# Kernel optimization log

Measured on AMD Instinct MI355X. Metric: run time of the kernel, lower is better.

## Reference

```python
import jax, jax.numpy as jnp
import numpy as np

B, H, L, T, V, LAYERS = 512, 256, 256, 64, 128, 2
SOS = 0


def setup_inputs() -> dict:
    key = jax.random.key(0)
    ks = jax.random.split(key, 10)
    s = 0.05
    return {
        "x": jax.random.normal(ks[0], (B, H, 1, L), jnp.float32),          # encoder memory
        "y": jax.random.randint(ks[1], (B, T), 0, V, jnp.int32),            # teacher tokens
        "emb": jax.random.normal(ks[2], (V, H), jnp.float32) * s,           # embedding table
        "attn_w": jax.random.normal(ks[3], (L, 2 * H), jnp.float32) * s,    # attn Linear [out,in]
        "attn_b": jnp.zeros((L,), jnp.float32),
        "comb_w": jax.random.normal(ks[4], (H, 2 * H), jnp.float32) * s,    # attn_combine
        "comb_b": jnp.zeros((H,), jnp.float32),
        "gru_w_ih": jax.random.normal(ks[5], (LAYERS, 3 * H, H), jnp.float32) * s,
        "gru_w_hh": jax.random.normal(ks[6], (LAYERS, 3 * H, H), jnp.float32) * s,
        "gru_b_ih": jnp.zeros((LAYERS, 3 * H), jnp.float32),
        "gru_b_hh": jnp.zeros((LAYERS, 3 * H), jnp.float32),
        "out_w": jax.random.normal(ks[7], (V, H), jnp.float32) * s,
        "out_b": jnp.zeros((V,), jnp.float32),
    }


def reference(x, y, emb, attn_w, attn_b, comb_w, comb_b,
              gru_w_ih, gru_w_hh, gru_b_ih, gru_b_hh, out_w, out_b):
    # x: [B, H, 1, L] -> encoder memory enc: [B, L, H]
    enc = jnp.transpose(x[:, :, 0, :], (0, 2, 1))
    b = x.shape[0]
    h0 = jnp.zeros((LAYERS, b, H), x.dtype)
    # teacher forcing: input at step t is y[:, t-1], with SOS at t=0
    tokens = jnp.concatenate([jnp.full((b, 1), SOS, y.dtype), y[:, :-1]], axis=1)  # [B, T]

    def step(hidden, tok):
        e = emb[tok]  # [B, H] (dropout disabled / eval mode)
        scores = jnp.concatenate([e, hidden[0]], axis=1) @ attn_w.T + attn_b  # [B, L]
        aw = jax.nn.softmax(scores, axis=1)
        applied = jnp.einsum('bl,blh->bh', aw, enc)  # [B, H]
        g = jax.nn.relu(jnp.concatenate([applied, e], axis=1) @ comb_w.T + comb_b)
        xin = g
        hs = []
        for l in range(LAYERS):  # single-step multilayer GRU (PyTorch equations)
            gi = xin @ gru_w_ih[l].T + gru_b_ih[l]
            gh = hidden[l] @ gru_w_hh[l].T + gru_b_hh[l]
            ir, iz, inn = jnp.split(gi, 3, axis=1)
            hr, hz, hn = jnp.split(gh, 3, axis=1)
            r = jax.nn.sigmoid(ir + hr)
            z = jax.nn.sigmoid(iz + hz)
            n = jnp.tanh(inn + r * hn)
            hnew = (1 - z) * n + z * hidden[l]
            hs.append(hnew)
            xin = hnew
        logp = jax.nn.log_softmax(xin @ out_w.T + out_b, axis=1)  # [B, V]
        return jnp.stack(hs), (logp, aw)

    _, (outs, attns) = jax.lax.scan(step, h0, tokens.T)  # outs: [T,B,V], attns: [T,B,L]
    return jnp.transpose(outs, (1, 2, 0)), jnp.transpose(attns, (1, 0, 2))
```

## Files before the change

### kernel.cpp

```cpp
#include <hip/hip_runtime.h>
#include <math.h>

#define B 512
#define H 256
#define L 256
#define T 64
#define V 128
#define LAYERS 2
#define SOS 0

#define OFF_A 0
#define OFF_C 131072
#define OFF_G 262144
#define GRU_LAYER_STRIDE (6 * 65536)
#define GRU_MAT_STRIDE 65536
#define OFF_O (OFF_G + LAYERS * GRU_LAYER_STRIDE)
#define WS_HALVES (OFF_O + 32768)
#define OFF_XT WS_HALVES
#define XT_B_STRIDE (32 * 256 * 8)
#define XT_HALVES ((size_t)B * XT_B_STRIDE)
#define WS_NEED_BYTES ((size_t)(OFF_XT + XT_HALVES) * 2)

typedef _Float16 half8 __attribute__((ext_vector_type(8)));
typedef _Float16 half2t __attribute__((ext_vector_type(2)));
typedef unsigned int u32x4 __attribute__((ext_vector_type(4)));
typedef float f32x4 __attribute__((ext_vector_type(4)));

__device__ __forceinline__ float fdot2(half2t a, half2t b, float c) {
#if __has_builtin(__builtin_amdgcn_fdot2)
    return __builtin_amdgcn_fdot2(a, b, c, false);
#else
    return c + (float)a[0] * (float)b[0] + (float)a[1] * (float)b[1];
#endif
}

union H8 {
    half8 v;
    half2t p[4];
    u32x4 u;
};

__device__ __forceinline__ half8 nt_load_h8(const _Float16* p) {
    H8 t;
    t.u = __builtin_nontemporal_load((const u32x4*)p);
    return t.v;
}

__device__ __forceinline__ float sigmoidf_(float v) {
    return 1.f / (1.f + __expf(-v));
}
__device__ __forceinline__ float fast_tanh(float v) {
    v = fminf(fmaxf(v, -15.f), 15.f);
    float e = __expf(-2.f * v);
    return (1.f - e) / (1.f + e);
}

__global__ void prep_pack(const float* __restrict__ attn_w,
                          const float* __restrict__ comb_w,
                          const float* __restrict__ gru_w_ih,
                          const float* __restrict__ gru_w_hh,
                          const float* __restrict__ out_w,
                          _Float16* __restrict__ ws) {
    int stride = gridDim.x * blockDim.x;
    for (int idx = blockIdx.x * blockDim.x + threadIdx.x; idx < WS_HALVES; idx += stride) {
        float val;
        if (idx < OFF_C) {
            int i = idx & 7, r = idx >> 3;
            int l = r & 255, k8 = r >> 8;
            val = attn_w[l * 512 + k8 * 8 + i];
        } else if (idx < OFF_G) {
            int e = idx - OFF_C;
            int i = e & 7, r = e >> 3;
            int hh = r & 255, k8 = r >> 8;
            val = comb_w[hh * 512 + k8 * 8 + i];
        } else if (idx < OFF_O) {
            int e = idx - OFF_G;
            int layer = e / GRU_LAYER_STRIDE;
            e -= layer * GRU_LAYER_STRIDE;
            int mat = e >> 16;
            e &= 65535;
            int i = e & 7, r = e >> 3;
            int j = r & 255, k8 = r >> 8;
            int k = k8 * 8 + i;
            const float* src = (mat < 3) ? gru_w_ih : gru_w_hh;
            int gate = (mat < 3) ? mat : mat - 3;
            val = src[layer * (768 * 256) + (gate * 256 + j) * 256 + k];
        } else {
            int e = idx - OFF_O;
            int i = e & 7, r = e >> 3;
            int v = r & 127, k8 = r >> 7;
            val = out_w[v * 256 + k8 * 8 + i];
        }
        ws[idx] = (_Float16)val;
    }
}

__global__ void prep_x(const float* __restrict__ x, _Float16* __restrict__ xt) {
    const int b = blockIdx.x;
    const int h = threadIdx.x;
    const float* xr = x + ((size_t)b * H + h) * L;
    _Float16* base = xt + (size_t)b * XT_B_STRIDE + h * 8;
#pragma unroll 4
    for (int k8 = 0; k8 < 32; ++k8) {
        float4 v0 = *(const float4*)(xr + k8 * 8);
        float4 v1 = *(const float4*)(xr + k8 * 8 + 4);
        half8 o;
        o[0] = (_Float16)v0.x; o[1] = (_Float16)v0.y;
        o[2] = (_Float16)v0.z; o[3] = (_Float16)v0.w;
        o[4] = (_Float16)v1.x; o[5] = (_Float16)v1.y;
        o[6] = (_Float16)v1.z; o[7] = (_Float16)v1.w;
        *(half8*)(base + k8 * 2048) = o;
    }
}

template <bool USE_XT>
__global__ __launch_bounds__(1024, 4) void decoder_kernel(
    const float* __restrict__ x,
    const int* __restrict__ y,
    const float* __restrict__ emb,
    const float* __restrict__ attn_b,
    const float* __restrict__ comb_b,
    const float* __restrict__ gru_b_ih,
    const float* __restrict__ gru_b_hh,
    const float* __restrict__ out_b,
    const _Float16* __restrict__ wsh,
    const _Float16* __restrict__ xt,
    float* __restrict__ out) {
    __shared__ __align__(16) _Float16 ehf[2][512];
    __shared__ __align__(16) _Float16 hfs[LAYERS][2][256];
    __shared__ __align__(16) float h32[LAYERS][2][256];
    __shared__ __align__(16) _Float16 apf[2][256];
    __shared__ __align__(16) _Float16 gfv[2][256];
    __shared__ __align__(16) _Float16 awf[2][256];
    __shared__ __align__(16) float aw32[2][256];
    __shared__ __align__(16) float pbuf[4][2][256];
    __shared__ __align__(16) float pgru[4][2][3][256];
    __shared__ __align__(16) float po[4][2][128];
    __shared__ __align__(16) float lgbuf[2][128][33];

    const int tid = threadIdx.x;
    const int G = tid >> 8;
    const int h = tid & 255;
    const int lane = tid & 63;
    const int w = tid >> 6;
    const int b0 = blockIdx.x * 2;

    const _Float16* AW = wsh + OFF_A;
    const _Float16* CW = wsh + OFF_C;
    const _Float16* OW = wsh + OFF_O;

    const float ab = attn_b[h];
    const float cb = comb_b[h];
    const float ob = out_b[h & 127];
    float b_ir[LAYERS], b_iz[LAYERS], b_in[LAYERS], b_hr[LAYERS], b_hz[LAYERS], b_hn[LAYERS];
#pragma unroll
    for (int l = 0; l < LAYERS; ++l) {
        b_ir[l] = gru_b_ih[l * 768 + h];
        b_iz[l] = gru_b_ih[l * 768 + 256 + h];
        b_in[l] = gru_b_ih[l * 768 + 512 + h];
        b_hr[l] = gru_b_hh[l * 768 + h];
        b_hz[l] = gru_b_hh[l * 768 + 256 + h];
        b_hn[l] = gru_b_hh[l * 768 + 512 + h];
    }

    if (G < 2) {
#pragma unroll
        for (int l = 0; l < LAYERS; ++l) {
            h32[l][G][h] = 0.f;
            hfs[l][G][h] = (_Float16)0.f;
        }
        ehf[G][256 + h] = (_Float16)0.f;
    }
    __syncthreads();

    for (int t = 0; t < T; ++t) {
        if (G < 2) {
            int tok = (t == 0) ? SOS : y[(b0 + G) * T + (t - 1)];
            ehf[G][h] = (_Float16)emb[tok * H + h];
        }
        __syncthreads();

        {
            float a00 = 0.f, a01 = 0.f, a10 = 0.f, a11 = 0.f;
            const _Float16* wp = AW + ((G * 16) << 11) + (h << 3);
            const _Float16* e0 = &ehf[0][G << 7];
            const _Float16* e1 = &ehf[1][G << 7];
#pragma unroll 4
            for (int k8 = 0; k8 < 16; ++k8) {
                H8 uw, u0, u1;
                uw.v = *(const half8*)(wp + (k8 << 11));
                u0.v = *(const half8*)(e0 + (k8 << 3));
                u1.v = *(const half8*)(e1 + (k8 << 3));
                a00 = fdot2(uw.p[0], u0.p[0], a00);
                a00 = fdot2(uw.p[1], u0.p[1], a00);
                a01 = fdot2(uw.p[2], u0.p[2], a01);
                a01 = fdot2(uw.p[3], u0.p[3], a01);
                a10 = fdot2(uw.p[0], u1.p[0], a10);
                a10 = fdot2(uw.p[1], u1.p[1], a10);
                a11 = fdot2(uw.p[2], u1.p[2], a11);
                a11 = fdot2(uw.p[3], u1.p[3], a11);
            }
            float bias = (G == 0) ? ab : 0.f;
            pbuf[G][0][h] = a00 + a01 + bias;
            pbuf[G][1][h] = a10 + a11 + bias;
        }
        __syncthreads();

        if (w < 2) {
            const int r = w;
            float s0 = pbuf[0][r][lane] + pbuf[1][r][lane] + pbuf[2][r][lane] + pbuf[3][r][lane];
            float s1 = pbuf[0][r][lane + 64] + pbuf[1][r][lane + 64] + pbuf[2][r][lane + 64] + pbuf[3][r][lane + 64];
            float s2 = pbuf[0][r][lane + 128] + pbuf[1][r][lane + 128] + pbuf[2][r][lane + 128] + pbuf[3][r][lane + 128];
            float s3 = pbuf[0][r][lane + 192] + pbuf[1][r][lane + 192] + pbuf[2][r][lane + 192] + pbuf[3][r][lane + 192];
            float m = fmaxf(fmaxf(s0, s1), fmaxf(s2, s3));
            for (int off = 32; off; off >>= 1) m = fmaxf(m, __shfl_xor(m, off));
            float e0 = __expf(s0 - m), e1 = __expf(s1 - m);
            float e2 = __expf(s2 - m), e3 = __expf(s3 - m);
            float s = e0 + e1 + e2 + e3;
            for (int off = 32; off; off >>= 1) s += __shfl_xor(s, off);
            float inv = 1.f / s;
            e0 *= inv; e1 *= inv; e2 *= inv; e3 *= inv;
            if (USE_XT) {
                awf[r][lane] = (_Float16)e0;
                awf[r][lane + 64] = (_Float16)e1;
                awf[r][lane + 128] = (_Float16)e2;
                awf[r][lane + 192] = (_Float16)e3;
            } else {
                aw32[r][lane] = e0;
                aw32[r][lane + 64] = e1;
                aw32[r][lane + 128] = e2;
                aw32[r][lane + 192] = e3;
            }
            float* outA = out + (size_t)B * V * T + ((size_t)(b0 + r) * T + t) * L;
            __builtin_nontemporal_store(e0, outA + lane);
            __builtin_nontemporal_store(e1, outA + lane + 64);
            __builtin_nontemporal_store(e2, outA + lane + 128);
            __builtin_nontemporal_store(e3, outA + lane + 192);
        }
        __syncthreads();

        {
            const int r = G & 1;
            const int q = G >> 1;
            if (USE_XT) {
                const _Float16* xrow = xt + (size_t)(b0 + r) * XT_B_STRIDE + (q << 15) + (h << 3);
                const _Float16* ap = &awf[r][q << 7];
                float a0 = 0.f, a1 = 0.f;
#pragma unroll 4
                for (int k8 = 0; k8 < 16; ++k8) {
                    H8 uw, ua;
                    uw.v = nt_load_h8(xrow + (k8 << 11));
                    ua.v = *(const half8*)(ap + (k8 << 3));
                    a0 = fdot2(uw.p[0], ua.p[0], a0);
                    a0 = fdot2(uw.p[1], ua.p[1], a0);
                    a1 = fdot2(uw.p[2], ua.p[2], a1);
                    a1 = fdot2(uw.p[3], ua.p[3], a1);
                }
                pbuf[G][0][h] = a0 + a1;
            } else {
                const float* xrow = x + ((size_t)(b0 + r) * H + h) * L + (q << 7);
                const float* ap = &aw32[r][q << 7];
                float a0 = 0.f, a1 = 0.f;
#pragma unroll 4
                for (int l = 0; l < 128; l += 8) {
                    float4 x0 = *(const float4*)(xrow + l);
                    float4 x1 = *(const float4*)(xrow + l + 4);
                    float4 w0 = *(const float4*)(ap + l);
                    float4 w1 = *(const float4*)(ap + l + 4);
                    a0 += x0.x * w0.x + x0.y * w0.y + x0.z * w0.z + x0.w * w0.w;
                    a1 += x1.x * w1.x + x1.y * w1.y + x1.z * w1.z + x1.w * w1.w;
                }
                pbuf[G][0][h] = a0 + a1;
            }
        }
        __syncthreads();

        if (G < 2) apf[G][h] = (_Float16)(pbuf[G][0][h] + pbuf[G + 2][0][h]);
        __syncthreads();

        {
            float a00 = 0.f, a01 = 0.f, a10 = 0.f, a11 = 0.f;
            const _Float16* wp = CW + ((G * 16) << 11) + (h << 3);
            const _Float16* i0 = (G < 2) ? &apf[0][G << 7] : &ehf[0][(G - 2) << 7];
            const _Float16* i1 = (G < 2) ? &apf[1][G << 7] : &ehf[1][(G - 2) << 7];
#pragma unroll 4
            for (int k8 = 0; k8 < 16; ++k8) {
                H8 uw, u0, u1;
                uw.v = *(const half8*)(wp + (k8 << 11));
                u0.v = *(const half8*)(i0 + (k8 << 3));
                u1.v = *(const half8*)(i1 + (k8 << 3));
                a00 = fdot2(uw.p[0], u0.p[0], a00);
                a00 = fdot2(uw.p[1], u0.p[1], a00);
                a01 = fdot2(uw.p[2], u0.p[2], a01);
                a01 = fdot2(uw.p[3], u0.p[3], a01);
                a10 = fdot2(uw.p[0], u1.p[0], a10);
                a10 = fdot2(uw.p[1], u1.p[1], a10);
                a11 = fdot2(uw.p[2], u1.p[2], a11);
                a11 = fdot2(uw.p[3], u1.p[3], a11);
            }
            pbuf[G][0][h] = a00 + a01;
            pbuf[G][1][h] = a10 + a11;
        }
        __syncthreads();
        if (G < 2)
            gfv[G][h] = (_Float16)fmaxf(
                pbuf[0][G][h] + pbuf[1][G][h] + pbuf[2][G][h] + pbuf[3][G][h] + cb, 0.f);
        __syncthreads();

#pragma unroll
        for (int layer = 0; layer < LAYERS; ++layer) {
            const int mh = G >> 1;
            const int kq = G & 1;
            const _Float16* GW = wsh + OFF_G + layer * GRU_LAYER_STRIDE +
                                 mh * 3 * GRU_MAT_STRIDE + ((kq * 16) << 11) + (h << 3);
            const _Float16* act0;
            const _Float16* act1;
            if (mh == 0) {
                act0 = ((layer == 0) ? &gfv[0][0] : &hfs[0][0][0]) + (kq << 7);
                act1 = ((layer == 0) ? &gfv[1][0] : &hfs[0][1][0]) + (kq << 7);
            } else {
                act0 = &hfs[layer][0][0] + (kq << 7);
                act1 = &hfs[layer][1][0] + (kq << 7);
            }
            float aA0 = 0.f, aB0 = 0.f, aC0 = 0.f, aA1 = 0.f, aB1 = 0.f, aC1 = 0.f;
#pragma unroll 4
            for (int k8 = 0; k8 < 16; ++k8) {
                H8 w0, w1, w2, u0, u1;
                const int off = k8 << 11;
                w0.v = *(const half8*)(GW + off);
                w1.v = *(const half8*)(GW + GRU_MAT_STRIDE + off);
                w2.v = *(const half8*)(GW + 2 * GRU_MAT_STRIDE + off);
                u0.v = *(const half8*)(act0 + (k8 << 3));
                u1.v = *(const half8*)(act1 + (k8 << 3));
#pragma unroll
                for (int p = 0; p < 4; ++p) {
                    aA0 = fdot2(w0.p[p], u0.p[p], aA0);
                    aB0 = fdot2(w1.p[p], u0.p[p], aB0);
                    aC0 = fdot2(w2.p[p], u0.p[p], aC0);
                    aA1 = fdot2(w0.p[p], u1.p[p], aA1);
                    aB1 = fdot2(w1.p[p], u1.p[p], aB1);
                    aC1 = fdot2(w2.p[p], u1.p[p], aC1);
                }
            }
            pgru[G][0][0][h] = aA0;
            pgru[G][0][1][h] = aB0;
            pgru[G][0][2][h] = aC0;
            pgru[G][1][0][h] = aA1;
            pgru[G][1][1][h] = aB1;
            pgru[G][1][2][h] = aC1;
            __syncthreads();
            if (G < 2) {
                const int r = G;
                float gi_r = pgru[0][r][0][h] + pgru[1][r][0][h];
                float gi_z = pgru[0][r][1][h] + pgru[1][r][1][h];
                float gi_n = pgru[0][r][2][h] + pgru[1][r][2][h];
                float gh_r = pgru[2][r][0][h] + pgru[3][r][0][h];
                float gh_z = pgru[2][r][1][h] + pgru[3][r][1][h];
                float gh_n = pgru[2][r][2][h] + pgru[3][r][2][h];
                float rr = sigmoidf_(gi_r + b_ir[layer] + gh_r + b_hr[layer]);
                float zz = sigmoidf_(gi_z + b_iz[layer] + gh_z + b_hz[layer]);
                float nn = fast_tanh(gi_n + b_in[layer] + rr * (gh_n + b_hn[layer]));
                float hnew = (1.f - zz) * nn + zz * h32[layer][r][h];
                h32[layer][r][h] = hnew;
                hfs[layer][r][h] = (_Float16)hnew;
                if (layer == 0) ehf[r][256 + h] = (_Float16)hnew;
            }
            __syncthreads();
        }

        {
            const int v = h & 127;
            const int r = h >> 7;
            const _Float16* hp = &hfs[1][r][0] + (G << 6);
            const _Float16* wp = OW + ((G * 8) << 10) + (v << 3);
            float a0 = 0.f, a1 = 0.f;
#pragma unroll 4
            for (int k8 = 0; k8 < 8; ++k8) {
                H8 uw, ua;
                uw.v = *(const half8*)(wp + (k8 << 10));
                ua.v = *(const half8*)(hp + (k8 << 3));
                a0 = fdot2(uw.p[0], ua.p[0], a0);
                a0 = fdot2(uw.p[1], ua.p[1], a0);
                a1 = fdot2(uw.p[2], ua.p[2], a1);
                a1 = fdot2(uw.p[3], ua.p[3], a1);
            }
            po[G][r][v] = a0 + a1 + ((G == 0) ? ob : 0.f);
        }
        __syncthreads();

        if (w < 2) {
            const int r = w;
            float l0 = po[0][r][lane] + po[1][r][lane] + po[2][r][lane] + po[3][r][lane];
            float l1 = po[0][r][lane + 64] + po[1][r][lane + 64] + po[2][r][lane + 64] + po[3][r][lane + 64];
            float m = fmaxf(l0, l1);
            for (int off = 32; off; off >>= 1) m = fmaxf(m, __shfl_xor(m, off));
            float s = __expf(l0 - m) + __expf(l1 - m);
            for (int off = 32; off; off >>= 1) s += __shfl_xor(s, off);
            float lse = m + __logf(s);
            lgbuf[r][lane][t & 31] = l0 - lse;
            lgbuf[r][lane + 64][t & 31] = l1 - lse;
        }

        if ((t & 31) == 31) {
            __syncthreads();
            const int tb = t & ~31;
#pragma unroll
            for (int c = 0; c < 2; ++c) {
                int fidx = c * 1024 + tid;
                int r = fidx >> 10;
                int rem = fidx & 1023;
                int v = rem >> 3;
                int tq = (rem & 7) << 2;
                f32x4 vec = {lgbuf[r][v][tq], lgbuf[r][v][tq + 1],
                             lgbuf[r][v][tq + 2], lgbuf[r][v][tq + 3]};
                float* dst = out + (size_t)(b0 + r) * V * T + (size_t)v * T + tb + tq;
                __builtin_nontemporal_store(vec, (f32x4*)dst);
            }
        }
    }
}

extern "C" void kernel_launch(void* const* d_in, const int* in_sizes, int n_in,
                              void* d_out, int out_size, void* d_ws, size_t ws_size,
                              hipStream_t stream) {
    const float* x = (const float*)d_in[0];
    const int* y = (const int*)d_in[1];
    const float* emb = (const float*)d_in[2];
    const float* attn_w = (const float*)d_in[3];
    const float* attn_b = (const float*)d_in[4];
    const float* comb_w = (const float*)d_in[5];
    const float* comb_b = (const float*)d_in[6];
    const float* gru_w_ih = (const float*)d_in[7];
    const float* gru_w_hh = (const float*)d_in[8];
    const float* gru_b_ih = (const float*)d_in[9];
    const float* gru_b_hh = (const float*)d_in[10];
    const float* out_w = (const float*)d_in[11];
    const float* out_b = (const float*)d_in[12];
    float* out = (float*)d_out;
    _Float16* ws = (_Float16*)d_ws;

    prep_pack<<<512, 256, 0, stream>>>(attn_w, comb_w, gru_w_ih, gru_w_hh, out_w, ws);
    if (ws_size >= WS_NEED_BYTES) {
        _Float16* xt = ws + OFF_XT;
        prep_x<<<B, 256, 0, stream>>>(x, xt);
        decoder_kernel<true><<<B / 2, 1024, 0, stream>>>(
            x, y, emb, attn_b, comb_b, gru_b_ih, gru_b_hh, out_b, ws, xt, out);
    } else {
        decoder_kernel<false><<<B / 2, 1024, 0, stream>>>(
            x, y, emb, attn_b, comb_b, gru_b_ih, gru_b_hh, out_b, ws, nullptr, out);
    }
}
```

Measured before the change: 2.087 ms.

## Process four batch rows per block to reuse weight loads across rows

Each workgroup now handles four sequences instead of two, so every packed fp16 weight vector loaded for the attention, combine, GRU and output projections is reused across four activation rows. Grid size halves to 128 blocks. The attention-apply step is reassigned so each 256-thread group covers a full row over all of L, which removes one reduction pass and a barrier. Costs are more LDS, more accumulator registers per thread, and fewer blocks than CUs, which can leave compute units idle. The logits flush now runs every 8 steps instead of every 32, and the host-side argument variables were shuffled, though the values passed stay the same.

```diff
diff --git a/kernel.cpp b/kernel.cpp
--- a/kernel.cpp
+++ b/kernel.cpp
@@ -126,24 +126,24 @@
     const _Float16* __restrict__ wsh,
     const _Float16* __restrict__ xt,
     float* __restrict__ out) {
-    __shared__ __align__(16) _Float16 ehf[2][512];
-    __shared__ __align__(16) _Float16 hfs[LAYERS][2][256];
-    __shared__ __align__(16) float h32[LAYERS][2][256];
-    __shared__ __align__(16) _Float16 apf[2][256];
-    __shared__ __align__(16) _Float16 gfv[2][256];
-    __shared__ __align__(16) _Float16 awf[2][256];
-    __shared__ __align__(16) float aw32[2][256];
-    __shared__ __align__(16) float pbuf[4][2][256];
-    __shared__ __align__(16) float pgru[4][2][3][256];
-    __shared__ __align__(16) float po[4][2][128];
-    __shared__ __align__(16) float lgbuf[2][128][33];
+    __shared__ __align__(16) _Float16 ehf[4][512];
+    __shared__ __align__(16) _Float16 hfs[LAYERS][4][256];
+    __shared__ __align__(16) float h32[LAYERS][4][256];
+    __shared__ __align__(16) _Float16 apf[4][256];
+    __shared__ __align__(16) _Float16 gfv[4][256];
+    __shared__ __align__(16) _Float16 awf[4][256];
+    __shared__ __align__(16) float aw32[4][256];
+    __shared__ __align__(16) float pbuf[4][4][256];
+    __shared__ __align__(16) float pgru[4][4][3][256];
+    __shared__ __align__(16) float po[4][4][128];
+    __shared__ __align__(16) float lgbuf[4][128][9];
 
     const int tid = threadIdx.x;
     const int G = tid >> 8;
     const int h = tid & 255;
     const int lane = tid & 63;
     const int w = tid >> 6;
-    const int b0 = blockIdx.x * 2;
+    const int b0 = blockIdx.x * 4;
 
     const _Float16* AW = wsh + OFF_A;
     const _Float16* CW = wsh + OFF_C;
@@ -151,7 +151,7 @@
 
     const float ab = attn_b[h];
     const float cb = comb_b[h];
-    const float ob = out_b[h & 127];
+    const float ob = out_b[tid & 127];
     float b_ir[LAYERS], b_iz[LAYERS], b_in[LAYERS], b_hr[LAYERS], b_hz[LAYERS], b_hn[LAYERS];
 #pragma unroll
     for (int l = 0; l < LAYERS; ++l) {
@@ -163,50 +163,53 @@
         b_hn[l] = gru_b_hh[l * 768 + 512 + h];
     }
 
-    if (G < 2) {
-#pragma unroll
-        for (int l = 0; l < LAYERS; ++l) {
-            h32[l][G][h] = 0.f;
-            hfs[l][G][h] = (_Float16)0.f;
-        }
-        ehf[G][256 + h] = (_Float16)0.f;
-    }
+#pragma unroll
+    for (int l = 0; l < LAYERS; ++l) {
+        h32[l][G][h] = 0.f;
+        hfs[l][G][h] = (_Float16)0.f;
+    }
+    ehf[G][256 + h] = (_Float16)0.f;
     __syncthreads();
 
     for (int t = 0; t < T; ++t) {
-        if (G < 2) {
+        {
             int tok = (t == 0) ? SOS : y[(b0 + G) * T + (t - 1)];
             ehf[G][h] = (_Float16)emb[tok * H + h];
         }
         __syncthreads();
 
         {
-            float a00 = 0.f, a01 = 0.f, a10 = 0.f, a11 = 0.f;
+            float a0 = 0.f, a1 = 0.f, a2 = 0.f, a3 = 0.f;
             const _Float16* wp = AW + ((G * 16) << 11) + (h << 3);
             const _Float16* e0 = &ehf[0][G << 7];
             const _Float16* e1 = &ehf[1][G << 7];
+            const _Float16* e2 = &ehf[2][G << 7];
+            const _Float16* e3 = &ehf[3][G << 7];
 #pragma unroll 4
             for (int k8 = 0; k8 < 16; ++k8) {
-                H8 uw, u0, u1;
+                H8 uw, u0, u1, u2, u3;
                 uw.v = *(const half8*)(wp + (k8 << 11));
                 u0.v = *(const half8*)(e0 + (k8 << 3));
                 u1.v = *(const half8*)(e1 + (k8 << 3));
-                a00 = fdot2(uw.p[0], u0.p[0], a00);
-                a00 = fdot2(uw.p[1], u0.p[1], a00);
-                a01 = fdot2(uw.p[2], u0.p[2], a01);
-                a01 = fdot2(uw.p[3], u0.p[3], a01);
-                a10 = fdot2(uw.p[0], u1.p[0], a10);
-                a10 = fdot2(uw.p[1], u1.p[1], a10);
-                a11 = fdot2(uw.p[2], u1.p[2], a11);
-                a11 = fdot2(uw.p[3], u1.p[3], a11);
+                u2.v = *(const half8*)(e2 + (k8 << 3));
+                u3.v = *(const half8*)(e3 + (k8 << 3));
+#pragma unroll
+                for (int p = 0; p < 4; ++p) {
+                    a0 = fdot2(uw.p[p], u0.p[p], a0);
+                    a1 = fdot2(uw.p[p], u1.p[p], a1);
+                    a2 = fdot2(uw.p[p], u2.p[p], a2);
+                    a3 = fdot2(uw.p[p], u3.p[p], a3);
+                }
             }
             float bias = (G == 0) ? ab : 0.f;
-            pbuf[G][0][h] = a00 + a01 + bias;
-            pbuf[G][1][h] = a10 + a11 + bias;
-        }
-        __syncthreads();
-
-        if (w < 2) {
+            pbuf[G][0][h] = a0 + bias;
+            pbuf[G][1][h] = a1 + bias;
+            pbuf[G][2][h] = a2 + bias;
+            pbuf[G][3][h] = a3 + bias;
+        }
+        __syncthreads();
+
+        if (w < 4) {
             const int r = w;
             float s0 = pbuf[0][r][lane] + pbuf[1][r][lane] + pbuf[2][r][lane] + pbuf[3][r][lane];
             float s1 = pbuf[0][r][lane + 64] + pbuf[1][r][lane + 64] + pbuf[2][r][lane + 64] + pbuf[3][r][lane + 64];
@@ -239,72 +242,69 @@
         }
         __syncthreads();
 
+        if (USE_XT) {
+            const _Float16* xrow = xt + (size_t)(b0 + G) * XT_B_STRIDE + (h << 3);
+            const _Float16* ap = &awf[G][0];
+            float a0 = 0.f, a1 = 0.f;
+#pragma unroll 4
+            for (int k8 = 0; k8 < 32; ++k8) {
+                H8 uw, ua;
+                uw.v = nt_load_h8(xrow + (k8 << 11));
+                ua.v = *(const half8*)(ap + (k8 << 3));
+                a0 = fdot2(uw.p[0], ua.p[0], a0);
+                a0 = fdot2(uw.p[1], ua.p[1], a0);
+                a1 = fdot2(uw.p[2], ua.p[2], a1);
+                a1 = fdot2(uw.p[3], ua.p[3], a1);
+            }
+            apf[G][h] = (_Float16)(a0 + a1);
+        } else {
+            const float* xrow = x + ((size_t)(b0 + G) * H + h) * L;
+            const float* ap = &aw32[G][0];
+            float a0 = 0.f, a1 = 0.f;
+#pragma unroll 4
+            for (int l = 0; l < L; l += 8) {
+                float4 x0 = *(const float4*)(xrow + l);
+                float4 x1 = *(const float4*)(xrow + l + 4);
+                float4 w0 = *(const float4*)(ap + l);
+                float4 w1 = *(const float4*)(ap + l + 4);
+                a0 += x0.x * w0.x + x0.y * w0.y + x0.z * w0.z + x0.w * w0.w;
+                a1 += x1.x * w1.x + x1.y * w1.y + x1.z * w1.z + x1.w * w1.w;
+            }
+            apf[G][h] = (_Float16)(a0 + a1);
+        }
+        __syncthreads();
+
         {
-            const int r = G & 1;
-            const int q = G >> 1;
-            if (USE_XT) {
-                const _Float16* xrow = xt + (size_t)(b0 + r) * XT_B_STRIDE + (q << 15) + (h << 3);
-                const _Float16* ap = &awf[r][q << 7];
-                float a0 = 0.f, a1 = 0.f;
-#pragma unroll 4
-                for (int k8 = 0; k8 < 16; ++k8) {
-                    H8 uw, ua;
-                    uw.v = nt_load_h8(xrow + (k8 << 11));
-                    ua.v = *(const half8*)(ap + (k8 << 3));
-                    a0 = fdot2(uw.p[0], ua.p[0], a0);
-                    a0 = fdot2(uw.p[1], ua.p[1], a0);
-                    a1 = fdot2(uw.p[2], ua.p[2], a1);
-                    a1 = fdot2(uw.p[3], ua.p[3], a1);
-                }
-                pbuf[G][0][h] = a0 + a1;
-            } else {
-                const float* xrow = x + ((size_t)(b0 + r) * H + h) * L + (q << 7);
-                const float* ap = &aw32[r][q << 7];
-                float a0 = 0.f, a1 = 0.f;
-#pragma unroll 4
-                for (int l = 0; l < 128; l += 8) {
-                    float4 x0 = *(const float4*)(xrow + l);
-                    float4 x1 = *(const float4*)(xrow + l + 4);
-                    float4 w0 = *(const float4*)(ap + l);
-                    float4 w1 = *(const float4*)(ap + l + 4);
-                    a0 += x0.x * w0.x + x0.y * w0.y + x0.z * w0.z + x0.w * w0.w;
-                    a1 += x1.x * w1.x + x1.y * w1.y + x1.z * w1.z + x1.w * w1.w;
-                }
-                pbuf[G][0][h] = a0 + a1;
-            }
-        }
-        __syncthreads();
-
-        if (G < 2) apf[G][h] = (_Float16)(pbuf[G][0][h] + pbuf[G + 2][0][h]);
-        __syncthreads();
-
-        {
-            float a00 = 0.f, a01 = 0.f, a10 = 0.f, a11 = 0.f;
+            float a0 = 0.f, a1 = 0.f, a2 = 0.f, a3 = 0.f;
             const _Float16* wp = CW + ((G * 16) << 11) + (h << 3);
             const _Float16* i0 = (G < 2) ? &apf[0][G << 7] : &ehf[0][(G - 2) << 7];
             const _Float16* i1 = (G < 2) ? &apf[1][G << 7] : &ehf[1][(G - 2) << 7];
+            const _Float16* i2 = (G < 2) ? &apf[2][G << 7] : &ehf[2][(G - 2) << 7];
+            const _Float16* i3 = (G < 2) ? &apf[3][G << 7] : &ehf[3][(G - 2) << 7];
 #pragma unroll 4
             for (int k8 = 0; k8 < 16; ++k8) {
-                H8 uw, u0, u1;
+                H8 uw, u0, u1, u2, u3;
                 uw.v = *(const half8*)(wp + (k8 << 11));
                 u0.v = *(const half8*)(i0 + (k8 << 3));
                 u1.v = *(const half8*)(i1 + (k8 << 3));
-                a00 = fdot2(uw.p[0], u0.p[0], a00);
-                a00 = fdot2(uw.p[1], u0.p[1], a00);
-                a01 = fdot2(uw.p[2], u0.p[2], a01);
-                a01 = fdot2(uw.p[3], u0.p[3], a01);
-                a10 = fdot2(uw.p[0], u1.p[0], a10);
-                a10 = fdot2(uw.p[1], u1.p[1], a10);
-                a11 = fdot2(uw.p[2], u1.p[2], a11);
-                a11 = fdot2(uw.p[3], u1.p[3], a11);
-            }
-            pbuf[G][0][h] = a00 + a01;
-            pbuf[G][1][h] = a10 + a11;
-        }
-        __syncthreads();
-        if (G < 2)
-            gfv[G][h] = (_Float16)fmaxf(
-                pbuf[0][G][h] + pbuf[1][G][h] + pbuf[2][G][h] + pbuf[3][G][h] + cb, 0.f);
+                u2.v = *(const half8*)(i2 + (k8 << 3));
+                u3.v = *(const half8*)(i3 + (k8 << 3));
+#pragma unroll
+                for (int p = 0; p < 4; ++p) {
+                    a0 = fdot2(uw.p[p], u0.p[p], a0);
+                    a1 = fdot2(uw.p[p], u1.p[p], a1);
+                    a2 = fdot2(uw.p[p], u2.p[p], a2);
+                    a3 = fdot2(uw.p[p], u3.p[p], a3);
+                }
+            }
+            pbuf[G][0][h] = a0;
+            pbuf[G][1][h] = a1;
+            pbuf[G][2][h] = a2;
+            pbuf[G][3][h] = a3;
+        }
+        __syncthreads();
+        gfv[G][h] = (_Float16)fmaxf(
+            pbuf[0][G][h] + pbuf[1][G][h] + pbuf[2][G][h] + pbuf[3][G][h] + cb, 0.f);
         __syncthreads();
 
 #pragma unroll
@@ -313,43 +313,44 @@
             const int kq = G & 1;
             const _Float16* GW = wsh + OFF_G + layer * GRU_LAYER_STRIDE +
                                  mh * 3 * GRU_MAT_STRIDE + ((kq * 16) << 11) + (h << 3);
-            const _Float16* act0;
-            const _Float16* act1;
-            if (mh == 0) {
-                act0 = ((layer == 0) ? &gfv[0][0] : &hfs[0][0][0]) + (kq << 7);
-                act1 = ((layer == 0) ? &gfv[1][0] : &hfs[0][1][0]) + (kq << 7);
-            } else {
-                act0 = &hfs[layer][0][0] + (kq << 7);
-                act1 = &hfs[layer][1][0] + (kq << 7);
-            }
-            float aA0 = 0.f, aB0 = 0.f, aC0 = 0.f, aA1 = 0.f, aB1 = 0.f, aC1 = 0.f;
-#pragma unroll 4
+            const _Float16* act[4];
+#pragma unroll
+            for (int r = 0; r < 4; ++r) {
+                if (mh == 0)
+                    act[r] = ((layer == 0) ? &gfv[r][0] : &hfs[0][r][0]) + (kq << 7);
+                else
+                    act[r] = &hfs[layer][r][0] + (kq << 7);
+            }
+            float aA[4] = {0.f, 0.f, 0.f, 0.f};
+            float aB[4] = {0.f, 0.f, 0.f, 0.f};
+            float aC[4] = {0.f, 0.f, 0.f, 0.f};
+#pragma unroll 2
             for (int k8 = 0; k8 < 16; ++k8) {
-                H8 w0, w1, w2, u0, u1;
+                H8 w0, w1, w2, u[4];
                 const int off = k8 << 11;
                 w0.v = *(const half8*)(GW + off);
                 w1.v = *(const half8*)(GW + GRU_MAT_STRIDE + off);
                 w2.v = *(const half8*)(GW + 2 * GRU_MAT_STRIDE + off);
-                u0.v = *(const half8*)(act0 + (k8 << 3));
-                u1.v = *(const half8*)(act1 + (k8 << 3));
+#pragma unroll
+                for (int r = 0; r < 4; ++r) u[r].v = *(const half8*)(act[r] + (k8 << 3));
 #pragma unroll
                 for (int p = 0; p < 4; ++p) {
-                    aA0 = fdot2(w0.p[p], u0.p[p], aA0);
-                    aB0 = fdot2(w1.p[p], u0.p[p], aB0);
-                    aC0 = fdot2(w2.p[p], u0.p[p], aC0);
-                    aA1 = fdot2(w0.p[p], u1.p[p], aA1);
-                    aB1 = fdot2(w1.p[p], u1.p[p], aB1);
-                    aC1 = fdot2(w2.p[p], u1.p[p], aC1);
+#pragma unroll
+                    for (int r = 0; r < 4; ++r) {
+                        aA[r] = fdot2(w0.p[p], u[r].p[p], aA[r]);
+                        aB[r] = fdot2(w1.p[p], u[r].p[p], aB[r]);
+                        aC[r] = fdot2(w2.p[p], u[r].p[p], aC[r]);
+                    }
                 }
             }
-            pgru[G][0][0][h] = aA0;
-            pgru[G][0][1][h] = aB0;
-            pgru[G][0][2][h] = aC0;
-            pgru[G][1][0][h] = aA1;
-            pgru[G][1][1][h] = aB1;
-            pgru[G][1][2][h] = aC1;
+#pragma unroll
+            for (int r = 0; r < 4; ++r) {
+                pgru[G][r][0][h] = aA[r];
+                pgru[G][r][1][h] = aB[r];
+                pgru[G][r][2][h] = aC[r];
+            }
             __syncthreads();
-            if (G < 2) {
+            {
                 const int r = G;
                 float gi_r = pgru[0][r][0][h] + pgru[1][r][0][h];
                 float gi_z = pgru[0][r][1][h] + pgru[1][r][1][h];
@@ -368,27 +369,36 @@
             __syncthreads();
         }
 
-        {
-            const int v = h & 127;
-            const int r = h >> 7;
-            const _Float16* hp = &hfs[1][r][0] + (G << 6);
-            const _Float16* wp = OW + ((G * 8) << 10) + (v << 3);
-            float a0 = 0.f, a1 = 0.f;
-#pragma unroll 4
+        if (tid < 512) {
+            const int v = tid & 127;
+            const int kq = tid >> 7;
+            const _Float16* wp = OW + ((kq * 8) << 10) + (v << 3);
+            float a0 = 0.f, a1 = 0.f, a2 = 0.f, a3 = 0.f;
+#pragma unroll 2
             for (int k8 = 0; k8 < 8; ++k8) {
-                H8 uw, ua;
+                H8 uw, u0, u1, u2, u3;
                 uw.v = *(const half8*)(wp + (k8 << 10));
-                ua.v = *(const half8*)(hp + (k8 << 3));
-                a0 = fdot2(uw.p[0], ua.p[0], a0);
-                a0 = fdot2(uw.p[1], ua.p[1], a0);
-                a1 = fdot2(uw.p[2], ua.p[2], a1);
-                a1 = fdot2(uw.p[3], ua.p[3], a1);
-            }
-            po[G][r][v] = a0 + a1 + ((G == 0) ? ob : 0.f);
-        }
-        __syncthreads();
-
-        if (w < 2) {
+                u0.v = *(const half8*)(&hfs[1][0][kq << 6] + (k8 << 3));
+                u1.v = *(const half8*)(&hfs[1][1][kq << 6] + (k8 << 3));
+                u2.v = *(const half8*)(&hfs[1][2][kq << 6] + (k8 << 3));
+                u3.v = *(const half8*)(&hfs[1][3][kq << 6] + (k8 << 3));
+#pragma unroll
+                for (int p = 0; p < 4; ++p) {
+                    a0 = fdot2(uw.p[p], u0.p[p], a0);
+                    a1 = fdot2(uw.p[p], u1.p[p], a1);
+                    a2 = fdot2(uw.p[p], u2.p[p], a2);
+                    a3 = fdot2(uw.p[p], u3.p[p], a3);
+                }
+            }
+            float bias = (kq == 0) ? ob : 0.f;
+            po[kq][0][v] = a0 + bias;
+            po[kq][1][v] = a1 + bias;
+            po[kq][2][v] = a2 + bias;
+            po[kq][3][v] = a3 + bias;
+        }
+        __syncthreads();
+
+        if (w < 4) {
             const int r = w;
             float l0 = po[0][r][lane] + po[1][r][lane] + po[2][r][lane] + po[3][r][lane];
             float l1 = po[0][r][lane + 64] + po[1][r][lane + 64] + po[2][r][lane + 64] + po[3][r][lane + 64];
@@ -397,25 +407,21 @@
             float s = __expf(l0 - m) + __expf(l1 - m);
             for (int off = 32; off; off >>= 1) s += __shfl_xor(s, off);
             float lse = m + __logf(s);
-            lgbuf[r][lane][t & 31] = l0 - lse;
-            lgbuf[r][lane + 64][t & 31] = l1 - lse;
-        }
-
-        if ((t & 31) == 31) {
+            lgbuf[r][lane][t & 7] = l0 - lse;
+            lgbuf[r][lane + 64][t & 7] = l1 - lse;
+        }
+
+        if ((t & 7) == 7) {
             __syncthreads();
-            const int tb = t & ~31;
-#pragma unroll
-            for (int c = 0; c < 2; ++c) {
-                int fidx = c * 1024 + tid;
-                int r = fidx >> 10;
-                int rem = fidx & 1023;
-                int v = rem >> 3;
-                int tq = (rem & 7) << 2;
-                f32x4 vec = {lgbuf[r][v][tq], lgbuf[r][v][tq + 1],
-                             lgbuf[r][v][tq + 2], lgbuf[r][v][tq + 3]};
-                float* dst = out + (size_t)(b0 + r) * V * T + (size_t)v * T + tb + tq;
-                __builtin_nontemporal_store(vec, (f32x4*)dst);
-            }
+            const int tb = t & ~7;
+            int r = tid >> 8;
+            int rem = tid & 255;
+            int v = rem >> 1;
+            int tq = (rem & 1) << 2;
+            f32x4 vec = {lgbuf[r][v][tq], lgbuf[r][v][tq + 1],
+                         lgbuf[r][v][tq + 2], lgbuf[r][v][tq + 3]};
+            float* dst = out + (size_t)(b0 + r) * V * T + (size_t)v * T + tb + tq;
+            __builtin_nontemporal_store(vec, (f32x4*)dst);
         }
     }
 }
@@ -426,10 +432,11 @@
     const float* x = (const float*)d_in[0];
     const int* y = (const int*)d_in[1];
     const float* emb = (const float*)d_in[2];
-    const float* attn_w = (const float*)d_in[3];
-    const float* attn_b = (const float*)d_in[4];
+    const float* attn_b = (const float*)d_in[3];
+    const float* comb_b = (const float*)d_in[6];
     const float* comb_w = (const float*)d_in[5];
-    const float* comb_b = (const float*)d_in[6];
+    const float* attn_w2 = (const float*)d_in[3];
+    const float* attn_b2 = (const float*)d_in[4];
     const float* gru_w_ih = (const float*)d_in[7];
     const float* gru_w_hh = (const float*)d_in[8];
     const float* gru_b_ih = (const float*)d_in[9];
@@ -439,14 +446,14 @@
     float* out = (float*)d_out;
     _Float16* ws = (_Float16*)d_ws;
 
-    prep_pack<<<512, 256, 0, stream>>>(attn_w, comb_w, gru_w_ih, gru_w_hh, out_w, ws);
+    prep_pack<<<512, 256, 0, stream>>>(attn_w2, comb_w, gru_w_ih, gru_w_hh, out_w, ws);
     if (ws_size >= WS_NEED_BYTES) {
         _Float16* xt = ws + OFF_XT;
         prep_x<<<B, 256, 0, stream>>>(x, xt);
-        decoder_kernel<true><<<B / 2, 1024, 0, stream>>>(
-            x, y, emb, attn_b, comb_b, gru_b_ih, gru_b_hh, out_b, ws, xt, out);
+        decoder_kernel<true><<<B / 4, 1024, 0, stream>>>(
+            x, y, emb, attn_b2, comb_b, gru_b_ih, gru_b_hh, out_b, ws, xt, out);
     } else {
-        decoder_kernel<false><<<B / 2, 1024, 0, stream>>>(
-            x, y, emb, attn_b, comb_b, gru_b_ih, gru_b_hh, out_b, ws, nullptr, out);
-    }
-}
+        decoder_kernel<false><<<B / 4, 1024, 0, stream>>>(
+            x, y, emb, attn_b2, comb_b, gru_b_ih, gru_b_hh, out_b, ws, nullptr, out);
+    }
+}
```

After: 2.656 ms. 27.2% more time.
